# Performance work log

Hardware: AMD Instinct MI355X
Metric: run time of the kernel (lower is better)

The kernel has to match this reference:

```python
import jax, jax.numpy as jnp
import numpy as np

N, E, H, C = 100000, 1600000, 64, 40

def _mlp(h, w1, b1, w2, b2):
    return jax.nn.relu(h @ w1 + b1) @ w2 + b2

def setup_inputs() -> dict:
    key = jax.random.key(0)
    ks = jax.random.split(key, 16)
    def w(k, shape, fan_in):
        return jax.random.normal(k, shape, jnp.float32) / np.sqrt(fan_in)
    return {
        "x": jax.random.normal(ks[0], (N, H), jnp.float32),
        "edge_index": jax.random.randint(ks[1], (2, E), 0, N, jnp.int64),
        "edge_attr": jax.random.normal(ks[2], (E, 1), jnp.float32),
        # edge_mlp: Linear(1,H) -> ReLU -> Linear(H,H)
        "e_w1": w(ks[3], (1, H), 1), "e_b1": jnp.zeros((H,), jnp.float32),
        "e_w2": w(ks[4], (H, H), H), "e_b2": jnp.zeros((H,), jnp.float32),
        # conv1 update MLP + eps
        "eps1": jnp.zeros((), jnp.float32),
        "m1_w1": w(ks[5], (H, H), H), "m1_b1": jnp.zeros((H,), jnp.float32),
        "m1_w2": w(ks[6], (H, H), H), "m1_b2": jnp.zeros((H,), jnp.float32),
        # conv2 update MLP + eps
        "eps2": jnp.zeros((), jnp.float32),
        "m2_w1": w(ks[7], (H, H), H), "m2_b1": jnp.zeros((H,), jnp.float32),
        "m2_w2": w(ks[8], (H, H), H), "m2_b2": jnp.zeros((H,), jnp.float32),
        # classifier
        "lin_w": w(ks[9], (H, C), H), "lin_b": jnp.zeros((C,), jnp.float32),
    }

def reference(x, edge_index, edge_attr, e_w1, e_b1, e_w2, e_b2,
              eps1, m1_w1, m1_b1, m1_w2, m1_b2,
              eps2, m2_w1, m2_b1, m2_w2, m2_b2, lin_w, lin_b):
    n = x.shape[0]
    src, dst = edge_index[0], edge_index[1]
    edge_emb = _mlp(edge_attr, e_w1, e_b1, e_w2, e_b2)  # [E, H]

    def gine_conv(h, eps, w1, b1, w2, b2):
        msg = jax.nn.relu(h[src] + edge_emb)                 # gather + fuse  [E, H]
        aggr = jax.ops.segment_sum(msg, dst, num_segments=n) # scatter-add   [N, H]
        return _mlp((1.0 + eps) * h + aggr, w1, b1, w2, b2)

    h = jax.nn.relu(gine_conv(x, eps1, m1_w1, m1_b1, m1_w2, m1_b2))
    # dropout is identity in eval mode
    h = jax.nn.relu(gine_conv(h, eps2, m2_w1, m2_b1, m2_w2, m2_b2))
    return jax.nn.log_softmax(h @ lin_w + lin_b, axis=1)
```

## Files before the change

### kernel.cpp

```cpp
#include <hip/hip_runtime.h>
#include <hip/hip_bf16.h>
#include <stdint.h>


typedef unsigned int uint32;
typedef unsigned short ushort16;
typedef __attribute__((ext_vector_type(8))) short bf16x8;
typedef __attribute__((ext_vector_type(4))) float f32x4;

#define BKT_SHIFT 9
#define BKT_SIZE 512
#define BKT_MASK 511
#define BSPLIT 4

static __device__ __forceinline__ unsigned short f2bf(float f) {
  __hip_bfloat16 h = __float2bfloat16(f);
  return *reinterpret_cast<unsigned short*>(&h);
}
static __device__ __forceinline__ float bf2f(unsigned short u) {
  return __uint_as_float(((uint32)u) << 16);
}

static __device__ __forceinline__ bool detect_is64(const uint32* ei, int E, int tid, int* sflag) {
  if (tid < 64) {
    int lim = (E < 64) ? E : 64;
    int nz = (tid < lim) ? (ei[2 * (size_t)tid + 1] != 0u) : 0;
    nz = __any(nz);
    if (tid == 0) *sflag = !nz;
  }
  __syncthreads();
  return *sflag != 0;
}

__global__ __launch_bounds__(256) void k_setup_cast_count(
    const float* __restrict__ w1, const float* __restrict__ b1,
    const float* __restrict__ w2, const float* __restrict__ b2,
    float* __restrict__ tsS, uint32* __restrict__ ABp,
    const float* __restrict__ xin, ushort16* __restrict__ xb, int n4,
    const uint32* __restrict__ ei, int* __restrict__ hist1, int E, int KB) {
  __shared__ float w2s[64 * 64];
  __shared__ float b2s[64];
  __shared__ float w1s[64], b1s[64], ts[64];
  __shared__ int rs[64], ms[64], vs[64];
  __shared__ int h[1024];
  __shared__ int sIs64;
  const int tid = threadIdx.x;
  const int CB = (n4 + 255) >> 8;
  if (blockIdx.x >= (uint32)(65 + CB)) {
    const int b = blockIdx.x - (65 + CB);
    for (int i = tid; i < 1024; i += 256) h[i] = 0;
    bool is64 = detect_is64(ei, E, tid, &sIs64);
    for (int i = b * 256 + tid; i < E; i += KB * 256) {
      int dst = is64 ? (int)ei[2 * ((size_t)E + i)] : (int)ei[(size_t)E + i];
      atomicAdd(&h[dst >> BKT_SHIFT], 1);
    }
    __syncthreads();
    for (int i = tid; i < 1024; i += 256)
      if (h[i]) atomicAdd(&hist1[i], h[i]);
    return;
  }
  if (blockIdx.x >= 65) {
    int i = (blockIdx.x - 65) * 256 + tid;
    if (i < n4) {
      float4 v = ((const float4*)xin)[i];
      ushort4 o;
      o.x = f2bf(v.x); o.y = f2bf(v.y); o.z = f2bf(v.z); o.w = f2bf(v.w);
      ((ushort4*)xb)[i] = o;
    }
    return;
  }
  const int p = blockIdx.x;
  {
    const float4* g4 = (const float4*)w2;
    float4* s4 = (float4*)w2s;
    for (int i = tid; i < 64 * 16; i += 256) s4[i] = g4[i];
    if (tid < 64) b2s[tid] = b2[tid];
  }
  if (tid < 64) {
    float w = w1[tid], b = b1[tid];
    w1s[tid] = w; b1s[tid] = b;
    int v = (w != 0.0f);
    vs[tid] = v;
    ts[tid] = v ? (-b / w) : 0.0f;
  }
  __syncthreads();
  if (tid < 64) {
    float tk = ts[tid];
    int r = 0, m = 0;
    for (int k = 0; k < 64; ++k) if (vs[k]) { r += (ts[k] < tk) ? 1 : 0; m += (ts[k] == tk) ? 1 : 0; }
    rs[tid] = r; ms[tid] = m;
    if (p == 0) {
      int pos;
      if (vs[tid]) {
        int c = 0;
        for (int j = 0; j < 64; ++j)
          if (vs[j] && (ts[j] < tk || (ts[j] == tk && j < tid))) c++;
        pos = c;
      } else {
        int c = 0;
        for (int j = 0; j < 64; ++j) if (vs[j]) c++;
        for (int j = 0; j < tid; ++j) if (!vs[j]) c++;
        pos = c;
      }
      tsS[pos] = vs[tid] ? tk : __builtin_inff();
    }
  }
  __syncthreads();
  if (tid < 64) {
    const int j = tid;
    float accA = 0.0f, accB = b2s[j];
    for (int k = 0; k < 64; ++k) {
      bool act;
      if (vs[k]) act = (w1s[k] > 0.0f) ? (p >= rs[k] + ms[k]) : (p <= rs[k]);
      else       act = (b1s[k] > 0.0f);
      if (act) { float wv = w2s[k * 64 + j]; accA = fmaf(w1s[k], wv, accA); accB = fmaf(b1s[k], wv, accB); }
    }
    ABp[p * 64 + j] = (uint32)f2bf(accA) | ((uint32)f2bf(accB) << 16);
  }
}

static __device__ __forceinline__ int scan_hist(const int* __restrict__ hist1,
                                                int* bo, int* psum, int tid) {
  int v0 = hist1[tid * 4 + 0], v1 = hist1[tid * 4 + 1];
  int v2 = hist1[tid * 4 + 2], v3 = hist1[tid * 4 + 3];
  int sum = v0 + v1 + v2 + v3;
  psum[tid] = sum;
  __syncthreads();
  for (int d = 1; d < 256; d <<= 1) {
    int add = (tid >= d) ? psum[tid - d] : 0;
    __syncthreads();
    psum[tid] += add;
    __syncthreads();
  }
  int run = psum[tid] - sum;
  bo[tid * 4 + 0] = run; run += v0;
  bo[tid * 4 + 1] = run; run += v1;
  bo[tid * 4 + 2] = run; run += v2;
  bo[tid * 4 + 3] = run; run += v3;
  int total = psum[255];
  __syncthreads();
  return total;
}


__global__ __launch_bounds__(256) void k_bpart(
    const uint32* __restrict__ ei, const float* __restrict__ ea,
    const float* __restrict__ tsSg, const int* __restrict__ hist1,
    int* __restrict__ bCur,
    int2* __restrict__ stage, unsigned short* __restrict__ dstw, int E) {
  __shared__ int cnt[1024];
  __shared__ int bo[1024];
  __shared__ int psum[256];
  __shared__ float tss[64];
  __shared__ int sIs64;
  __shared__ int2 sspay[2048];
  __shared__ uint32 ssmeta[2048];
  const int tid = threadIdx.x;
  for (int i = tid; i < 1024; i += 256) cnt[i] = 0;
  if (tid >= 64 && tid < 128) tss[tid - 64] = tsSg[tid - 64];
  bool is64 = detect_is64(ei, E, tid, &sIs64);
  scan_hist(hist1, bo, psum, tid);
  const int base0 = blockIdx.x * 2048;
  int dstv[8], srcv[8], rk[8];
  float av[8];
#pragma unroll
  for (int e = 0; e < 8; ++e) {
    int idx = base0 + e * 256 + tid;
    if (idx < E) {
      int src, dst;
      if (is64) { src = (int)ei[2 * (size_t)idx]; dst = (int)ei[2 * ((size_t)E + idx)]; }
      else      { src = (int)ei[(size_t)idx];     dst = (int)ei[(size_t)E + idx]; }
      dstv[e] = dst; srcv[e] = src; av[e] = ea[idx];
      rk[e] = atomicAdd(&cnt[dst >> BKT_SHIFT], 1);
    } else dstv[e] = -1;
  }
  __syncthreads();
  for (int b = tid; b < 1024; b += 256) {
    int c = cnt[b];
    if (c) bo[b] = bo[b] + atomicAdd(&bCur[b], c);
  }
  int v0 = cnt[tid * 4 + 0], v1 = cnt[tid * 4 + 1];
  int v2 = cnt[tid * 4 + 2], v3 = cnt[tid * 4 + 3];
  int lsum = v0 + v1 + v2 + v3;
  __syncthreads();
  psum[tid] = lsum;
  __syncthreads();
  for (int d = 1; d < 256; d <<= 1) {
    int add = (tid >= d) ? psum[tid - d] : 0;
    __syncthreads();
    psum[tid] += add;
    __syncthreads();
  }
  int lrun = psum[tid] - lsum;
  cnt[tid * 4 + 0] = lrun; lrun += v0;
  cnt[tid * 4 + 1] = lrun; lrun += v1;
  cnt[tid * 4 + 2] = lrun; lrun += v2;
  cnt[tid * 4 + 3] = lrun;
  const int totloc = psum[255];
  __syncthreads();
#pragma unroll
  for (int e = 0; e < 8; ++e) {
    if (dstv[e] < 0) continue;
    float a = av[e];
    int p = 0;
#pragma unroll
    for (int s = 32; s > 0; s >>= 1) if (tss[p + s - 1] < a) p += s;
    if (tss[p] < a) ++p;
    const int b = dstv[e] >> BKT_SHIFT;
    const int slot = cnt[b] + rk[e];
    const int gd = bo[b] + rk[e];
    sspay[slot] = make_int2(srcv[e] | (p << 20), __float_as_int(a));
    ssmeta[slot] = (uint32)gd | ((uint32)(dstv[e] & BKT_MASK) << 21);
  }
  __syncthreads();
  for (int j = tid; j < totloc; j += 256) {
    uint32 m = ssmeta[j];
    int gd = (int)(m & 0x1FFFFFu);
    stage[gd] = sspay[j];
    dstw[gd] = (unsigned short)(m >> 21);
  }
}

__global__ __launch_bounds__(256) void k_blocal(
    const int* __restrict__ hist1, const int2* __restrict__ stage,
    const unsigned short* __restrict__ dstw,
    int* __restrict__ offs, int2* __restrict__ pay, int N) {
  __shared__ int bo[1024];
  __shared__ int psum[256];
  __shared__ int h[512], cur[512], ps2[256];
  const int tid = threadIdx.x;
  const int b = blockIdx.x >> 2;
  const int sub = blockIdx.x & 3;
  const int nbkt = (int)gridDim.x >> 2;
  int Etot = scan_hist(hist1, bo, psum, tid);
  const int s = bo[b];
  const int e2 = (b == nbkt - 1) ? Etot : bo[b + 1];
  if (b == 0 && sub == 0 && tid == 0) offs[N] = Etot;
  h[tid] = 0; h[tid + 256] = 0;
  __syncthreads();
  for (int j = s + tid; j < e2; j += 256) atomicAdd(&h[dstw[j]], 1);
  __syncthreads();
  int a0 = h[2 * tid], a1 = h[2 * tid + 1];
  ps2[tid] = a0 + a1;
  __syncthreads();
  for (int d = 1; d < 256; d <<= 1) {
    int add = (tid >= d) ? ps2[tid - d] : 0;
    __syncthreads();
    ps2[tid] += add;
    __syncthreads();
  }
  int ex = s + ps2[tid] - (a0 + a1);
  cur[2 * tid] = ex;
  cur[2 * tid + 1] = ex + a0;
  {
    int local = 2 * tid;
    if ((local >> 7) == sub) {
      int nd0 = b * BKT_SIZE + local;
      if (nd0 < N) offs[nd0] = ex;
      if (nd0 + 1 < N) offs[nd0 + 1] = ex + a0;
    }
  }
  __syncthreads();
  const int lo = sub << 7, hi = lo + 128;
  for (int j = s + tid; j < e2; j += 256) {
    int d = dstw[j];
    if (d >= lo && d < hi) {
      int pos = atomicAdd(&cur[d], 1);
      pay[pos] = stage[j];
    }
  }
}


#define EDGE8_LOAD(ib, qx, av)                                   \
  _Pragma("unroll")                                              \
  for (int t = 0; t < 8; ++t) {                                  \
    int2 q_ = pay[(ib) + t];                                     \
    qx[t] = (uint32)__builtin_amdgcn_readfirstlane(q_.x);        \
    av[t] = (uint32)__builtin_amdgcn_readfirstlane(q_.y);        \
  }

#define EDGE8_GATHER(qx, xv, ab)                                 \
  _Pragma("unroll")                                              \
  for (int t = 0; t < 8; ++t) {                                  \
    xv[t] = bf2f(xb[(size_t)(qx[t] & 0xFFFFFu) * 64u + lane]);   \
    ab[t] = ABs[(qx[t] >> 20) * 64u + lane];                     \
  }

#define EDGE8_ACC(av, xv, ab, acc)                               \
  _Pragma("unroll")                                              \
  for (int t = 0; t < 8; ++t)                                    \
    acc += fmaxf(fmaf(__uint_as_float(av[t]),                    \
                      __uint_as_float(ab[t] << 16),              \
                      __uint_as_float(ab[t] & 0xffff0000u)) + xv[t], 0.0f);

#define EDGE1(ib, acc) do {                                      \
    int2 q_ = pay[(ib)];                                         \
    uint32 qx_ = (uint32)__builtin_amdgcn_readfirstlane(q_.x);   \
    uint32 av_ = (uint32)__builtin_amdgcn_readfirstlane(q_.y);   \
    float xv_ = bf2f(xb[(size_t)(qx_ & 0xFFFFFu) * 64u + lane]); \
    uint32 ab_ = ABs[(qx_ >> 20) * 64u + lane];                  \
    acc += fmaxf(fmaf(__uint_as_float(av_),                      \
                      __uint_as_float(ab_ << 16),                \
                      __uint_as_float(ab_ & 0xffff0000u)) + xv_, 0.0f); \
  } while (0)

__global__ __launch_bounds__(512, 8) void k_conv(
    const unsigned short* __restrict__ xb,
    const int* __restrict__ offs, const int2* __restrict__ pay,
    const uint32* __restrict__ ABp, const float* __restrict__ epsp,
    unsigned short* __restrict__ uout, int n) {
  __shared__ uint32 ABs[65 * 64];
  {
    const uint4* g4 = (const uint4*)ABp;
    uint4* s4 = (uint4*)ABs;
    for (int i = threadIdx.x; i < 65 * 16; i += 512) s4[i] = g4[i];
  }
  __syncthreads();
  const int lane = threadIdx.x & 63;
  const int wid = __builtin_amdgcn_readfirstlane((int)(threadIdx.x >> 6));
  const float scale = 1.0f + epsp[0];
  const int npair = (n + 1) >> 1;
  for (int w = blockIdx.x * 8 + wid; w < npair; w += gridDim.x * 8) {
    const int ndA = __builtin_amdgcn_readfirstlane(w * 2);
    const bool hasB = (ndA + 1) < n;
    const int sA = offs[ndA];
    const int eA = offs[ndA + 1];
    const int eB = hasB ? offs[ndA + 2] : eA;
    float accA = 0.0f, accB = 0.0f;
    int iA = sA, iB = eA;
    while (iA + 7 < eA && iB + 7 < eB) {
      const int ia = __builtin_amdgcn_readfirstlane(iA);
      const int ib = __builtin_amdgcn_readfirstlane(iB);
      uint32 qxA[8], avA[8], qxB[8], avB[8];
      EDGE8_LOAD(ia, qxA, avA);
      EDGE8_LOAD(ib, qxB, avB);
      float xvA[8], xvB[8];
      uint32 abA[8], abB[8];
      EDGE8_GATHER(qxA, xvA, abA);
      EDGE8_GATHER(qxB, xvB, abB);
      EDGE8_ACC(avA, xvA, abA, accA);
      EDGE8_ACC(avB, xvB, abB, accB);
      iA += 8; iB += 8;
    }
    while (iA + 7 < eA) {
      const int ia = __builtin_amdgcn_readfirstlane(iA);
      uint32 qx[8], av[8];
      EDGE8_LOAD(ia, qx, av);
      float xv[8]; uint32 ab[8];
      EDGE8_GATHER(qx, xv, ab);
      EDGE8_ACC(av, xv, ab, accA);
      iA += 8;
    }
    while (iB + 7 < eB) {
      const int ib = __builtin_amdgcn_readfirstlane(iB);
      uint32 qx[8], av[8];
      EDGE8_LOAD(ib, qx, av);
      float xv[8]; uint32 ab[8];
      EDGE8_GATHER(qx, xv, ab);
      EDGE8_ACC(av, xv, ab, accB);
      iB += 8;
    }
    while (iA < eA && iB < eB) {
      const int ia = __builtin_amdgcn_readfirstlane(iA);
      const int ib = __builtin_amdgcn_readfirstlane(iB);
      int2 qa = pay[ia];
      int2 qb = pay[ib];
      uint32 qxa = (uint32)__builtin_amdgcn_readfirstlane(qa.x);
      uint32 ava = (uint32)__builtin_amdgcn_readfirstlane(qa.y);
      uint32 qxb = (uint32)__builtin_amdgcn_readfirstlane(qb.x);
      uint32 avb = (uint32)__builtin_amdgcn_readfirstlane(qb.y);
      float xva = bf2f(xb[(size_t)(qxa & 0xFFFFFu) * 64u + lane]);
      float xvb = bf2f(xb[(size_t)(qxb & 0xFFFFFu) * 64u + lane]);
      uint32 aba = ABs[(qxa >> 20) * 64u + lane];
      uint32 abb = ABs[(qxb >> 20) * 64u + lane];
      accA += fmaxf(fmaf(__uint_as_float(ava), __uint_as_float(aba << 16),
                         __uint_as_float(aba & 0xffff0000u)) + xva, 0.0f);
      accB += fmaxf(fmaf(__uint_as_float(avb), __uint_as_float(abb << 16),
                         __uint_as_float(abb & 0xffff0000u)) + xvb, 0.0f);
      ++iA; ++iB;
    }
    while (iA < eA) { EDGE1(__builtin_amdgcn_readfirstlane(iA), accA); ++iA; }
    while (iB < eB) { EDGE1(__builtin_amdgcn_readfirstlane(iB), accB); ++iB; }
    float xsA = bf2f(xb[(size_t)ndA * 64 + lane]);
    uout[(size_t)ndA * 64 + lane] = f2bf(fmaf(scale, xsA, accA));
    if (hasB) {
      float xsB = bf2f(xb[((size_t)ndA + 1) * 64 + lane]);
      uout[((size_t)ndA + 1) * 64 + lane] = f2bf(fmaf(scale, xsB, accB));
    }
  }
}

template <int OUTW>
static __device__ __forceinline__ bf16x8 load_bfrag(const float* __restrict__ W,
                                                    int hh, int q, int ncol, bool valid) {
  bf16x8 f;
#pragma unroll
  for (int j = 0; j < 8; ++j) {
    int k = hh * 32 + q * 8 + j;
    f[j] = valid ? (short)f2bf(W[k * OUTW + ncol]) : (short)0;
  }
  return f;
}

#define MFMA_BF16(A, B, C) __builtin_amdgcn_mfma_f32_16x16x32_bf16((A), (B), (C), 0, 0, 0)

__global__ __launch_bounds__(256) void k_mlp1(
    const unsigned short* __restrict__ uin, unsigned short* __restrict__ houtb,
    const float* __restrict__ W1, const float* __restrict__ B1,
    const float* __restrict__ W2, const float* __restrict__ B2, int n) {
  __shared__ unsigned short T[4][16 * 72];
  const int lane = threadIdx.x & 63;
  const int wid = threadIdx.x >> 6;
  const int cl = lane & 15;
  const int q = lane >> 4;
  bf16x8 w1f[4][2], w2f[4][2];
  float b1v[4], b2v[4];
#pragma unroll
  for (int t = 0; t < 4; ++t) {
#pragma unroll
    for (int hh = 0; hh < 2; ++hh) {
      w1f[t][hh] = load_bfrag<64>(W1, hh, q, t * 16 + cl, true);
      w2f[t][hh] = load_bfrag<64>(W2, hh, q, t * 16 + cl, true);
    }
    b1v[t] = B1[t * 16 + cl];
    b2v[t] = B2[t * 16 + cl];
  }
  unsigned short* Tw = T[wid];
  for (int node0 = blockIdx.x * 64 + wid * 16; node0 < n; node0 += gridDim.x * 64) {
    const unsigned short* ub = uin + (size_t)(node0 + cl) * 64;
    bf16x8 au0 = *(const bf16x8*)(ub + q * 8);
    bf16x8 au1 = *(const bf16x8*)(ub + 32 + q * 8);
#pragma unroll
    for (int t = 0; t < 4; ++t) {
      f32x4 acc = {b1v[t], b1v[t], b1v[t], b1v[t]};
      acc = MFMA_BF16(au0, w1f[t][0], acc);
      acc = MFMA_BF16(au1, w1f[t][1], acc);
#pragma unroll
      for (int r = 0; r < 4; ++r)
        Tw[(q * 4 + r) * 72 + t * 16 + cl] = f2bf(fmaxf(acc[r], 0.0f));
    }
    bf16x8 ah0 = *(const bf16x8*)&Tw[cl * 72 + q * 8];
    bf16x8 ah1 = *(const bf16x8*)&Tw[cl * 72 + 32 + q * 8];
#pragma unroll
    for (int t = 0; t < 4; ++t) {
      f32x4 acc = {b2v[t], b2v[t], b2v[t], b2v[t]};
      acc = MFMA_BF16(ah0, w2f[t][0], acc);
      acc = MFMA_BF16(ah1, w2f[t][1], acc);
#pragma unroll
      for (int r = 0; r < 4; ++r)
        Tw[(q * 4 + r) * 72 + t * 16 + cl] = f2bf(fmaxf(acc[r], 0.0f));
    }
    int m2 = lane >> 2, pt = lane & 3;
    if (node0 + m2 < n) {
      bf16x8 c0 = *(const bf16x8*)&Tw[m2 * 72 + pt * 16];
      bf16x8 c1 = *(const bf16x8*)&Tw[m2 * 72 + pt * 16 + 8];
      unsigned short* ob = houtb + (size_t)(node0 + m2) * 64 + pt * 16;
      *(bf16x8*)ob = c0;
      *(bf16x8*)(ob + 8) = c1;
    }
  }
}

__global__ __launch_bounds__(256) void k_mlp_cls(
    const unsigned short* __restrict__ uin,
    const float* __restrict__ W1, const float* __restrict__ B1,
    const float* __restrict__ W2, const float* __restrict__ B2,
    const float* __restrict__ LW, const float* __restrict__ LB,
    float* __restrict__ out, int n) {
  __shared__ unsigned short T[4][16 * 72];
  __shared__ float L[4][16 * 52];
  const int lane = threadIdx.x & 63;
  const int wid = threadIdx.x >> 6;
  const int cl = lane & 15;
  const int q = lane >> 4;
  bf16x8 w1f[4][2], w2f[4][2], lwf[3][2];
  float b1v[4], b2v[4], lbv[3];
#pragma unroll
  for (int t = 0; t < 4; ++t) {
#pragma unroll
    for (int hh = 0; hh < 2; ++hh) {
      w1f[t][hh] = load_bfrag<64>(W1, hh, q, t * 16 + cl, true);
      w2f[t][hh] = load_bfrag<64>(W2, hh, q, t * 16 + cl, true);
    }
    b1v[t] = B1[t * 16 + cl];
    b2v[t] = B2[t * 16 + cl];
  }
#pragma unroll
  for (int t = 0; t < 3; ++t) {
    bool valid = (t * 16 + cl) < 40;
#pragma unroll
    for (int hh = 0; hh < 2; ++hh)
      lwf[t][hh] = load_bfrag<40>(LW, hh, q, valid ? (t * 16 + cl) : 0, valid);
    lbv[t] = valid ? LB[t * 16 + cl] : 0.0f;
  }
  unsigned short* Tw = T[wid];
  float* Lw = L[wid];
  for (int node0 = blockIdx.x * 64 + wid * 16; node0 < n; node0 += gridDim.x * 64) {
    const unsigned short* ub = uin + (size_t)(node0 + cl) * 64;
    bf16x8 au0 = *(const bf16x8*)(ub + q * 8);
    bf16x8 au1 = *(const bf16x8*)(ub + 32 + q * 8);
#pragma unroll
    for (int t = 0; t < 4; ++t) {
      f32x4 acc = {b1v[t], b1v[t], b1v[t], b1v[t]};
      acc = MFMA_BF16(au0, w1f[t][0], acc);
      acc = MFMA_BF16(au1, w1f[t][1], acc);
#pragma unroll
      for (int r = 0; r < 4; ++r)
        Tw[(q * 4 + r) * 72 + t * 16 + cl] = f2bf(fmaxf(acc[r], 0.0f));
    }
    bf16x8 ah0 = *(const bf16x8*)&Tw[cl * 72 + q * 8];
    bf16x8 ah1 = *(const bf16x8*)&Tw[cl * 72 + 32 + q * 8];
#pragma unroll
    for (int t = 0; t < 4; ++t) {
      f32x4 acc = {b2v[t], b2v[t], b2v[t], b2v[t]};
      acc = MFMA_BF16(ah0, w2f[t][0], acc);
      acc = MFMA_BF16(ah1, w2f[t][1], acc);
#pragma unroll
      for (int r = 0; r < 4; ++r)
        Tw[(q * 4 + r) * 72 + t * 16 + cl] = f2bf(fmaxf(acc[r], 0.0f));
    }
    bf16x8 g0 = *(const bf16x8*)&Tw[cl * 72 + q * 8];
    bf16x8 g1 = *(const bf16x8*)&Tw[cl * 72 + 32 + q * 8];
#pragma unroll
    for (int t = 0; t < 3; ++t) {
      f32x4 acc = {lbv[t], lbv[t], lbv[t], lbv[t]};
      acc = MFMA_BF16(g0, lwf[t][0], acc);
      acc = MFMA_BF16(g1, lwf[t][1], acc);
#pragma unroll
      for (int r = 0; r < 4; ++r)
        Lw[(q * 4 + r) * 52 + t * 16 + cl] = acc[r];
    }
    int m3 = lane >> 2, j3 = lane & 3;
    float lg[10];
#pragma unroll
    for (int i = 0; i < 10; ++i) lg[i] = Lw[m3 * 52 + j3 * 10 + i];
    float mx = lg[0];
#pragma unroll
    for (int i = 1; i < 10; ++i) mx = fmaxf(mx, lg[i]);
    mx = fmaxf(mx, __shfl_xor(mx, 1));
    mx = fmaxf(mx, __shfl_xor(mx, 2));
    float se = 0.0f;
#pragma unroll
    for (int i = 0; i < 10; ++i) se += __expf(lg[i] - mx);
    se += __shfl_xor(se, 1);
    se += __shfl_xor(se, 2);
    float lse = mx + __logf(se);
    if (node0 + m3 < n) {
      float* o = out + (size_t)(node0 + m3) * 40 + j3 * 10;
#pragma unroll
      for (int i = 0; i < 10; ++i) o[i] = lg[i] - lse;
    }
  }
}

extern "C" void kernel_launch(void* const* d_in, const int* in_sizes, int n_in,
                              void* d_out, int out_size, void* d_ws, size_t ws_size,
                              hipStream_t stream) {
  (void)n_in; (void)out_size; (void)ws_size;
  const float* x     = (const float*)d_in[0];
  const uint32* ei   = (const uint32*)d_in[1];
  const float* eattr = (const float*)d_in[2];
  const float* e_w1 = (const float*)d_in[3];
  const float* e_b1 = (const float*)d_in[4];
  const float* e_w2 = (const float*)d_in[5];
  const float* e_b2 = (const float*)d_in[6];
  const float* eps1 = (const float*)d_in[7];
  const float* m1w1 = (const float*)d_in[8];
  const float* m1b1 = (const float*)d_in[9];
  const float* m1w2 = (const float*)d_in[10];
  const float* m1b2 = (const float*)d_in[11];
  const float* eps2 = (const float*)d_in[12];
  const float* m2w1 = (const float*)d_in[13];
  const float* m2b1 = (const float*)d_in[14];
  const float* m2w2 = (const float*)d_in[15];
  const float* m2b2 = (const float*)d_in[16];
  const float* linw = (const float*)d_in[17];
  const float* linb = (const float*)d_in[18];

  const int N = in_sizes[0] / 64;
  const int E = in_sizes[1] / 2;
  const int NBKT = (N + BKT_SIZE - 1) >> BKT_SHIFT;

  char* ws = (char*)d_ws;
  size_t off = 0;
  auto alloc = [&](size_t bytes, size_t align) {
    off = (off + align - 1) & ~(align - 1);
    size_t r = off; off += bytes; return r;
  };
  size_t oT    = alloc(64 * 4, 64);
  size_t oAB   = alloc(65 * 64 * 4, 64);
  size_t oHC   = alloc(2048 * 4, 128);
  size_t oOffs = alloc(((size_t)N + 1) * 4, 128);
  size_t oPay  = alloc((size_t)E * 8, 256);
  size_t oXb   = alloc((size_t)N * 64 * 2 + 32768, 256);
  size_t oU    = alloc((size_t)N * 64 * 2 + 32768, 1024);
  size_t oStg  = alloc((size_t)E * 8, 256);
  size_t oDw   = alloc((size_t)E * 2, 256);

  float*  tsS  = (float*)(ws + oT);
  uint32* ABp  = (uint32*)(ws + oAB);
  int*    h1   = (int*)(ws + oHC);
  int*    bCur = (int*)(ws + oHC + 1024 * 4);
  int*    offs = (int*)(ws + oOffs);
  int2*   pay  = (int2*)(ws + oPay);
  ushort16* xb = (ushort16*)(ws + oXb);
  ushort16* ubuf = (ushort16*)(ws + oU);
  int2*   stage = (int2*)(ws + oStg);
  unsigned short* dstw = (unsigned short*)(ws + oDw);

  hipMemsetAsync(ws + oHC, 0, 2048 * 4, stream);

  const int n4 = N * 64 / 4;
  const int CB = (n4 + 255) / 256;
  const int PB = (E + 2047) / 2048;
  const int KB = 1024;
  const int MB = (N + 127) / 128;

  k_setup_cast_count<<<65 + CB + KB, 256, 0, stream>>>(
      e_w1, e_b1, e_w2, e_b2, tsS, ABp, x, xb, n4, ei, h1, E, KB);
  k_bpart<<<PB, 256, 0, stream>>>(ei, eattr, tsS, h1, bCur, stage, dstw, E);
  k_blocal<<<NBKT * BSPLIT, 256, 0, stream>>>(h1, stage, dstw, offs, pay, N);
  k_conv<<<1024, 512, 0, stream>>>((const unsigned short*)xb, offs, pay, ABp, eps1, ubuf, N);
  k_mlp1<<<MB, 256, 0, stream>>>((const unsigned short*)ubuf, (unsigned short*)xb,
                                 m1w1, m1b1, m1w2, m1b2, N);
  k_conv<<<1024, 512, 0, stream>>>((const unsigned short*)xb, offs, pay, ABp, eps2, ubuf, N);
  k_mlp_cls<<<MB, 256, 0, stream>>>((const unsigned short*)ubuf,
                                    m2w1, m2b1, m2w2, m2b2, linw, linb,
                                    (float*)d_out, N);
}
```

Measured before the change: 319.9 us.

## Fuse CSR-build setup, histogram, partition and local sort into one cooperative kernel

Replaces the memset plus three preprocessing kernels (setup/cast/count, bucket partition, bucket-local sort) with one persistent cooperative kernel. Its phases are separated by grid-wide syncs and walk the work with grid-stride loops. The goal is to remove launch gaps and the separate memset. In exchange it pays for grid.sync barriers, caps the grid at the number of co-resident blocks, and falls back to the old path when occupancy is too low.

```diff
diff --git a/kernel.cpp b/kernel.cpp
--- a/kernel.cpp
+++ b/kernel.cpp
@@ -1,6 +1,9 @@
 #include <hip/hip_runtime.h>
+#include <hip/hip_cooperative_groups.h>
 #include <hip/hip_bf16.h>
 #include <stdint.h>
+
+namespace cg = cooperative_groups;
 
 
 typedef unsigned int uint32;
@@ -30,6 +33,260 @@
   }
   __syncthreads();
   return *sflag != 0;
+}
+
+static __device__ __forceinline__ int scan_hist_p(const int* __restrict__ hist1,
+                                                  int* bo, int* psum, int tid) {
+  int v0 = hist1[tid * 4 + 0], v1 = hist1[tid * 4 + 1];
+  int v2 = hist1[tid * 4 + 2], v3 = hist1[tid * 4 + 3];
+  int sum = v0 + v1 + v2 + v3;
+  psum[tid] = sum;
+  __syncthreads();
+  for (int d = 1; d < 256; d <<= 1) {
+    int add = (tid >= d) ? psum[tid - d] : 0;
+    __syncthreads();
+    psum[tid] += add;
+    __syncthreads();
+  }
+  int run = psum[tid] - sum;
+  bo[tid * 4 + 0] = run; run += v0;
+  bo[tid * 4 + 1] = run; run += v1;
+  bo[tid * 4 + 2] = run; run += v2;
+  bo[tid * 4 + 3] = run; run += v3;
+  int total = psum[255];
+  __syncthreads();
+  return total;
+}
+
+__global__ __launch_bounds__(256, 4) void k_csr(
+    const float* __restrict__ w1, const float* __restrict__ b1,
+    const float* __restrict__ w2, const float* __restrict__ b2,
+    float* __restrict__ tsS, uint32* __restrict__ ABp,
+    const float* __restrict__ xin, ushort16* __restrict__ xb, int n4,
+    const uint32* __restrict__ ei, const float* __restrict__ ea,
+    int* __restrict__ hist1, int* __restrict__ bCur,
+    int2* __restrict__ stage, unsigned short* __restrict__ dstw,
+    int* __restrict__ offs, int2* __restrict__ pay, int N, int E) {
+  cg::grid_group grid = cg::this_grid();
+  const int tid = threadIdx.x;
+  const int bid = blockIdx.x;
+  const int G = (int)gridDim.x;
+  __shared__ __align__(16) char smem[34816];
+
+  if (bid < 65) {
+    float* w2s = (float*)smem;
+    float* b2s = (float*)(smem + 16384);
+    float* w1s = (float*)(smem + 16640);
+    float* b1s = (float*)(smem + 16896);
+    float* ts  = (float*)(smem + 17152);
+    int* rs = (int*)(smem + 17408);
+    int* ms = (int*)(smem + 17664);
+    int* vs = (int*)(smem + 17920);
+    const int p = bid;
+    {
+      const float4* g4 = (const float4*)w2;
+      float4* s4 = (float4*)w2s;
+      for (int i = tid; i < 64 * 16; i += 256) s4[i] = g4[i];
+      if (tid < 64) b2s[tid] = b2[tid];
+    }
+    if (tid < 64) {
+      float w = w1[tid], b = b1[tid];
+      w1s[tid] = w; b1s[tid] = b;
+      int v = (w != 0.0f);
+      vs[tid] = v;
+      ts[tid] = v ? (-b / w) : 0.0f;
+    }
+    __syncthreads();
+    if (tid < 64) {
+      float tk = ts[tid];
+      int r = 0, m = 0;
+      for (int k = 0; k < 64; ++k) if (vs[k]) { r += (ts[k] < tk) ? 1 : 0; m += (ts[k] == tk) ? 1 : 0; }
+      rs[tid] = r; ms[tid] = m;
+      if (p == 0) {
+        int pos;
+        if (vs[tid]) {
+          int c = 0;
+          for (int j = 0; j < 64; ++j)
+            if (vs[j] && (ts[j] < tk || (ts[j] == tk && j < tid))) c++;
+          pos = c;
+        } else {
+          int c = 0;
+          for (int j = 0; j < 64; ++j) if (vs[j]) c++;
+          for (int j = 0; j < tid; ++j) if (!vs[j]) c++;
+          pos = c;
+        }
+        tsS[pos] = vs[tid] ? tk : __builtin_inff();
+      }
+    }
+    __syncthreads();
+    if (tid < 64) {
+      const int j = tid;
+      float accA = 0.0f, accB = b2s[j];
+      for (int k = 0; k < 64; ++k) {
+        bool act;
+        if (vs[k]) act = (w1s[k] > 0.0f) ? (p >= rs[k] + ms[k]) : (p <= rs[k]);
+        else       act = (b1s[k] > 0.0f);
+        if (act) { float wv = w2s[k * 64 + j]; accA = fmaf(w1s[k], wv, accA); accB = fmaf(b1s[k], wv, accB); }
+      }
+      ABp[p * 64 + j] = (uint32)f2bf(accA) | ((uint32)f2bf(accB) << 16);
+    }
+  } else {
+    if (bid == G - 1) {
+      for (int i = tid; i < 2048; i += 256) hist1[i] = 0;
+    }
+    for (int i = (bid - 65) * 256 + tid; i < n4; i += (G - 65) * 256) {
+      float4 v = ((const float4*)xin)[i];
+      ushort4 o;
+      o.x = f2bf(v.x); o.y = f2bf(v.y); o.z = f2bf(v.z); o.w = f2bf(v.w);
+      ((ushort4*)xb)[i] = o;
+    }
+  }
+  grid.sync();
+
+  {
+    int* h = (int*)smem;
+    int* sflag = (int*)(smem + 4096);
+    for (int i = tid; i < 1024; i += 256) h[i] = 0;
+    bool is64 = detect_is64(ei, E, tid, sflag);
+    for (int i = bid * 256 + tid; i < E; i += G * 256) {
+      int dst = is64 ? (int)ei[2 * ((size_t)E + i)] : (int)ei[(size_t)E + i];
+      atomicAdd(&h[dst >> BKT_SHIFT], 1);
+    }
+    __syncthreads();
+    for (int i = tid; i < 1024; i += 256)
+      if (h[i]) atomicAdd(&hist1[i], h[i]);
+  }
+  grid.sync();
+
+  {
+    int* cnt = (int*)smem;
+    int* bo = (int*)(smem + 4096);
+    int* psum = (int*)(smem + 8192);
+    float* tss = (float*)(smem + 9216);
+    int* sflag = (int*)(smem + 9472);
+    int2* sspay = (int2*)(smem + 9728);
+    uint32* ssmeta = (uint32*)(smem + 26112);
+    if (tid >= 64 && tid < 128) tss[tid - 64] = tsS[tid - 64];
+    bool is64 = detect_is64(ei, E, tid, sflag);
+    const int PB = (E + 2047) >> 11;
+    for (int c = bid; c < PB; c += G) {
+      for (int i = tid; i < 1024; i += 256) cnt[i] = 0;
+      scan_hist_p(hist1, bo, psum, tid);
+      const int base0 = c * 2048;
+      int dstv[8], srcv[8], rk[8];
+      float av[8];
+#pragma unroll
+      for (int e = 0; e < 8; ++e) {
+        int idx = base0 + e * 256 + tid;
+        if (idx < E) {
+          int src, dst;
+          if (is64) { src = (int)ei[2 * (size_t)idx]; dst = (int)ei[2 * ((size_t)E + idx)]; }
+          else      { src = (int)ei[(size_t)idx];     dst = (int)ei[(size_t)E + idx]; }
+          dstv[e] = dst; srcv[e] = src; av[e] = ea[idx];
+          rk[e] = atomicAdd(&cnt[dst >> BKT_SHIFT], 1);
+        } else dstv[e] = -1;
+      }
+      __syncthreads();
+      for (int b = tid; b < 1024; b += 256) {
+        int cc = cnt[b];
+        if (cc) bo[b] = bo[b] + atomicAdd(&bCur[b], cc);
+      }
+      int v0 = cnt[tid * 4 + 0], v1 = cnt[tid * 4 + 1];
+      int v2 = cnt[tid * 4 + 2], v3 = cnt[tid * 4 + 3];
+      int lsum = v0 + v1 + v2 + v3;
+      __syncthreads();
+      psum[tid] = lsum;
+      __syncthreads();
+      for (int d = 1; d < 256; d <<= 1) {
+        int add = (tid >= d) ? psum[tid - d] : 0;
+        __syncthreads();
+        psum[tid] += add;
+        __syncthreads();
+      }
+      int lrun = psum[tid] - lsum;
+      cnt[tid * 4 + 0] = lrun; lrun += v0;
+      cnt[tid * 4 + 1] = lrun; lrun += v1;
+      cnt[tid * 4 + 2] = lrun; lrun += v2;
+      cnt[tid * 4 + 3] = lrun;
+      const int totloc = psum[255];
+      __syncthreads();
+#pragma unroll
+      for (int e = 0; e < 8; ++e) {
+        if (dstv[e] < 0) continue;
+        float a = av[e];
+        int p = 0;
+#pragma unroll
+        for (int s = 32; s > 0; s >>= 1) if (tss[p + s - 1] < a) p += s;
+        if (tss[p] < a) ++p;
+        const int b = dstv[e] >> BKT_SHIFT;
+        const int slot = cnt[b] + rk[e];
+        const int gd = bo[b] + rk[e];
+        sspay[slot] = make_int2(srcv[e] | (p << 20), __float_as_int(a));
+        ssmeta[slot] = (uint32)gd | ((uint32)(dstv[e] & BKT_MASK) << 21);
+      }
+      __syncthreads();
+      for (int j = tid; j < totloc; j += 256) {
+        uint32 m = ssmeta[j];
+        int gd = (int)(m & 0x1FFFFFu);
+        stage[gd] = sspay[j];
+        dstw[gd] = (unsigned short)(m >> 21);
+      }
+      __syncthreads();
+    }
+  }
+  grid.sync();
+
+  {
+    int* bo = (int*)smem;
+    int* psum = (int*)(smem + 4096);
+    int* h = (int*)(smem + 5120);
+    int* cur = (int*)(smem + 7168);
+    int* ps2 = (int*)(smem + 9216);
+    const int nbkt = (N + BKT_SIZE - 1) >> BKT_SHIFT;
+    const int S = nbkt * BSPLIT;
+    for (int s = bid; s < S; s += G) {
+      const int b = s >> 2;
+      const int sub = s & 3;
+      int Etot = scan_hist_p(hist1, bo, psum, tid);
+      const int sB = bo[b];
+      const int e2 = (b == nbkt - 1) ? Etot : bo[b + 1];
+      if (s == 0 && tid == 0) offs[N] = Etot;
+      h[tid] = 0; h[tid + 256] = 0;
+      __syncthreads();
+      for (int j = sB + tid; j < e2; j += 256) atomicAdd(&h[dstw[j]], 1);
+      __syncthreads();
+      int a0 = h[2 * tid], a1 = h[2 * tid + 1];
+      ps2[tid] = a0 + a1;
+      __syncthreads();
+      for (int d = 1; d < 256; d <<= 1) {
+        int add = (tid >= d) ? ps2[tid - d] : 0;
+        __syncthreads();
+        ps2[tid] += add;
+        __syncthreads();
+      }
+      int ex = sB + ps2[tid] - (a0 + a1);
+      cur[2 * tid] = ex;
+      cur[2 * tid + 1] = ex + a0;
+      {
+        int local = 2 * tid;
+        if ((local >> 7) == sub) {
+          int nd0 = b * BKT_SIZE + local;
+          if (nd0 < N) offs[nd0] = ex;
+          if (nd0 + 1 < N) offs[nd0 + 1] = ex + a0;
+        }
+      }
+      __syncthreads();
+      const int lo = sub << 7, hi = lo + 128;
+      for (int j = sB + tid; j < e2; j += 256) {
+        int d = dstw[j];
+        if (d >= lo && d < hi) {
+          int pos = atomicAdd(&cur[d], 1);
+          pay[pos] = stage[j];
+        }
+      }
+      __syncthreads();
+    }
+  }
 }
 
 __global__ __launch_bounds__(256) void k_setup_cast_count(
@@ -119,30 +376,6 @@
   }
 }
 
-static __device__ __forceinline__ int scan_hist(const int* __restrict__ hist1,
-                                                int* bo, int* psum, int tid) {
-  int v0 = hist1[tid * 4 + 0], v1 = hist1[tid * 4 + 1];
-  int v2 = hist1[tid * 4 + 2], v3 = hist1[tid * 4 + 3];
-  int sum = v0 + v1 + v2 + v3;
-  psum[tid] = sum;
-  __syncthreads();
-  for (int d = 1; d < 256; d <<= 1) {
-    int add = (tid >= d) ? psum[tid - d] : 0;
-    __syncthreads();
-    psum[tid] += add;
-    __syncthreads();
-  }
-  int run = psum[tid] - sum;
-  bo[tid * 4 + 0] = run; run += v0;
-  bo[tid * 4 + 1] = run; run += v1;
-  bo[tid * 4 + 2] = run; run += v2;
-  bo[tid * 4 + 3] = run; run += v3;
-  int total = psum[255];
-  __syncthreads();
-  return total;
-}
-
-
 __global__ __launch_bounds__(256) void k_bpart(
     const uint32* __restrict__ ei, const float* __restrict__ ea,
     const float* __restrict__ tsSg, const int* __restrict__ hist1,
@@ -159,7 +392,7 @@
   for (int i = tid; i < 1024; i += 256) cnt[i] = 0;
   if (tid >= 64 && tid < 128) tss[tid - 64] = tsSg[tid - 64];
   bool is64 = detect_is64(ei, E, tid, &sIs64);
-  scan_hist(hist1, bo, psum, tid);
+  scan_hist_p(hist1, bo, psum, tid);
   const int base0 = blockIdx.x * 2048;
   int dstv[8], srcv[8], rk[8];
   float av[8];
@@ -232,7 +465,7 @@
   const int b = blockIdx.x >> 2;
   const int sub = blockIdx.x & 3;
   const int nbkt = (int)gridDim.x >> 2;
-  int Etot = scan_hist(hist1, bo, psum, tid);
+  int Etot = scan_hist_p(hist1, bo, psum, tid);
   const int s = bo[b];
   const int e2 = (b == nbkt - 1) ? Etot : bo[b + 1];
   if (b == 0 && sub == 0 && tid == 0) offs[N] = Etot;
@@ -270,7 +503,6 @@
     }
   }
 }
-
 
 #define EDGE8_LOAD(ib, qx, av)                                   \
   _Pragma("unroll")                                              \
@@ -609,18 +841,43 @@
   int2*   stage = (int2*)(ws + oStg);
   unsigned short* dstw = (unsigned short*)(ws + oDw);
 
-  hipMemsetAsync(ws + oHC, 0, 2048 * 4, stream);
-
   const int n4 = N * 64 / 4;
   const int CB = (n4 + 255) / 256;
   const int PB = (E + 2047) / 2048;
   const int KB = 1024;
   const int MB = (N + 127) / 128;
 
-  k_setup_cast_count<<<65 + CB + KB, 256, 0, stream>>>(
-      e_w1, e_b1, e_w2, e_b2, tsS, ABp, x, xb, n4, ei, h1, E, KB);
-  k_bpart<<<PB, 256, 0, stream>>>(ei, eattr, tsS, h1, bCur, stage, dstw, E);
-  k_blocal<<<NBKT * BSPLIT, 256, 0, stream>>>(h1, stage, dstw, offs, pay, N);
+  static int g_coopG = -2;
+  if (g_coopG == -2) {
+    int mb = 0;
+    hipError_t err = hipOccupancyMaxActiveBlocksPerMultiprocessor(&mb, k_csr, 256, 0);
+    if (err != hipSuccess) mb = 0;
+    int g = mb * 256;
+    if (g > 1024) g = 1024;
+    g_coopG = (g >= 512) ? g : -1;
+  }
+
+  if (g_coopG > 0) {
+    int Nv = N, Ev = E, n4v = n4;
+    void* args[] = {
+      (void*)&e_w1, (void*)&e_b1, (void*)&e_w2, (void*)&e_b2,
+      (void*)&tsS, (void*)&ABp,
+      (void*)&x, (void*)&xb, (void*)&n4v,
+      (void*)&ei, (void*)&eattr,
+      (void*)&h1, (void*)&bCur,
+      (void*)&stage, (void*)&dstw,
+      (void*)&offs, (void*)&pay, (void*)&Nv, (void*)&Ev
+    };
+    hipLaunchCooperativeKernel((const void*)k_csr, dim3(g_coopG), dim3(256),
+                               args, 0, stream);
+  } else {
+    hipMemsetAsync(ws + oHC, 0, 2048 * 4, stream);
+    k_setup_cast_count<<<65 + CB + KB, 256, 0, stream>>>(
+        e_w1, e_b1, e_w2, e_b2, tsS, ABp, x, xb, n4, ei, h1, E, KB);
+    k_bpart<<<PB, 256, 0, stream>>>(ei, eattr, tsS, h1, bCur, stage, dstw, E);
+    k_blocal<<<NBKT * BSPLIT, 256, 0, stream>>>(h1, stage, dstw, offs, pay, N);
+  }
+
   k_conv<<<1024, 512, 0, stream>>>((const unsigned short*)xb, offs, pay, ABp, eps1, ubuf, N);
   k_mlp1<<<MB, 256, 0, stream>>>((const unsigned short*)ubuf, (unsigned short*)xb,
                                  m1w1, m1b1, m1w2, m1b2, N);
```

Result: slower. 683.5 us (+113.7%).

## Fuse GINE aggregation with following MLP into one kernel per layer

Applied to the files above, without the earlier changes.

Merges each conv aggregation kernel with the following MLP kernel. Every wave now aggregates 16 nodes, writes the results to shared memory, and runs the MFMA MLP on them directly. This removes the round trip of the intermediate u buffer through global memory and saves two launches. In exchange, register pressure rises, the launch bound drops to 4 blocks per CU, and each block now does one tile instead of grid-striding.

```diff
diff --git a/kernel.cpp b/kernel.cpp
--- a/kernel.cpp
+++ b/kernel.cpp
@@ -142,7 +142,6 @@
   return total;
 }
 
-
 __global__ __launch_bounds__(256) void k_bpart(
     const uint32* __restrict__ ei, const float* __restrict__ ea,
     const float* __restrict__ tsSg, const int* __restrict__ hist1,
@@ -271,7 +270,6 @@
   }
 }
 
-
 #define EDGE8_LOAD(ib, qx, av)                                   \
   _Pragma("unroll")                                              \
   for (int t = 0; t < 8; ++t) {                                  \
@@ -305,111 +303,99 @@
                       __uint_as_float(ab_ & 0xffff0000u)) + xv_, 0.0f); \
   } while (0)
 
-__global__ __launch_bounds__(512, 8) void k_conv(
+static __device__ __forceinline__ void conv_pair(
+    const unsigned short* __restrict__ xb, const int* __restrict__ offs,
+    const int2* __restrict__ pay, const uint32* ABs, const int lane,
+    const int ndA, const bool hasB, float& accA, float& accB) {
+  const int sA = offs[ndA];
+  const int eA = offs[ndA + 1];
+  const int eB = hasB ? offs[ndA + 2] : eA;
+  accA = 0.0f; accB = 0.0f;
+  int iA = sA, iB = eA;
+  while (iA + 7 < eA && iB + 7 < eB) {
+    const int ia = __builtin_amdgcn_readfirstlane(iA);
+    const int ib = __builtin_amdgcn_readfirstlane(iB);
+    uint32 qxA[8], avA[8], qxB[8], avB[8];
+    EDGE8_LOAD(ia, qxA, avA);
+    EDGE8_LOAD(ib, qxB, avB);
+    float xvA[8], xvB[8];
+    uint32 abA[8], abB[8];
+    EDGE8_GATHER(qxA, xvA, abA);
+    EDGE8_GATHER(qxB, xvB, abB);
+    EDGE8_ACC(avA, xvA, abA, accA);
+    EDGE8_ACC(avB, xvB, abB, accB);
+    iA += 8; iB += 8;
+  }
+  while (iA + 7 < eA) {
+    const int ia = __builtin_amdgcn_readfirstlane(iA);
+    uint32 qx[8], av[8];
+    EDGE8_LOAD(ia, qx, av);
+    float xv[8]; uint32 ab[8];
+    EDGE8_GATHER(qx, xv, ab);
+    EDGE8_ACC(av, xv, ab, accA);
+    iA += 8;
+  }
+  while (iB + 7 < eB) {
+    const int ib = __builtin_amdgcn_readfirstlane(iB);
+    uint32 qx[8], av[8];
+    EDGE8_LOAD(ib, qx, av);
+    float xv[8]; uint32 ab[8];
+    EDGE8_GATHER(qx, xv, ab);
+    EDGE8_ACC(av, xv, ab, accB);
+    iB += 8;
+  }
+  while (iA < eA && iB < eB) {
+    const int ia = __builtin_amdgcn_readfirstlane(iA);
+    const int ib = __builtin_amdgcn_readfirstlane(iB);
+    int2 qa = pay[ia];
+    int2 qb = pay[ib];
+    uint32 qxa = (uint32)__builtin_amdgcn_readfirstlane(qa.x);
+    uint32 ava = (uint32)__builtin_amdgcn_readfirstlane(qa.y);
+    uint32 qxb = (uint32)__builtin_amdgcn_readfirstlane(qb.x);
+    uint32 avb = (uint32)__builtin_amdgcn_readfirstlane(qb.y);
+    float xva = bf2f(xb[(size_t)(qxa & 0xFFFFFu) * 64u + lane]);
+    float xvb = bf2f(xb[(size_t)(qxb & 0xFFFFFu) * 64u + lane]);
+    uint32 aba = ABs[(qxa >> 20) * 64u + lane];
+    uint32 abb = ABs[(qxb >> 20) * 64u + lane];
+    accA += fmaxf(fmaf(__uint_as_float(ava), __uint_as_float(aba << 16),
+                       __uint_as_float(aba & 0xffff0000u)) + xva, 0.0f);
+    accB += fmaxf(fmaf(__uint_as_float(avb), __uint_as_float(abb << 16),
+                       __uint_as_float(abb & 0xffff0000u)) + xvb, 0.0f);
+    ++iA; ++iB;
+  }
+  while (iA < eA) { EDGE1(__builtin_amdgcn_readfirstlane(iA), accA); ++iA; }
+  while (iB < eB) { EDGE1(__builtin_amdgcn_readfirstlane(iB), accB); ++iB; }
+}
+
+template <int OUTW>
+static __device__ __forceinline__ bf16x8 load_bfrag(const float* __restrict__ W,
+                                                    int hh, int q, int ncol, bool valid) {
+  bf16x8 f;
+#pragma unroll
+  for (int j = 0; j < 8; ++j) {
+    int k = hh * 32 + q * 8 + j;
+    f[j] = valid ? (short)f2bf(W[k * OUTW + ncol]) : (short)0;
+  }
+  return f;
+}
+
+#define MFMA_BF16(A, B, C) __builtin_amdgcn_mfma_f32_16x16x32_bf16((A), (B), (C), 0, 0, 0)
+
+__global__ __launch_bounds__(512, 4) void k_conv_mlp1(
     const unsigned short* __restrict__ xb,
     const int* __restrict__ offs, const int2* __restrict__ pay,
     const uint32* __restrict__ ABp, const float* __restrict__ epsp,
-    unsigned short* __restrict__ uout, int n) {
+    const float* __restrict__ W1, const float* __restrict__ B1,
+    const float* __restrict__ W2, const float* __restrict__ B2,
+    unsigned short* __restrict__ hout, int n) {
   __shared__ uint32 ABs[65 * 64];
+  __shared__ unsigned short Tu[8][16 * 72];
   {
     const uint4* g4 = (const uint4*)ABp;
     uint4* s4 = (uint4*)ABs;
     for (int i = threadIdx.x; i < 65 * 16; i += 512) s4[i] = g4[i];
   }
   __syncthreads();
-  const int lane = threadIdx.x & 63;
-  const int wid = __builtin_amdgcn_readfirstlane((int)(threadIdx.x >> 6));
-  const float scale = 1.0f + epsp[0];
-  const int npair = (n + 1) >> 1;
-  for (int w = blockIdx.x * 8 + wid; w < npair; w += gridDim.x * 8) {
-    const int ndA = __builtin_amdgcn_readfirstlane(w * 2);
-    const bool hasB = (ndA + 1) < n;
-    const int sA = offs[ndA];
-    const int eA = offs[ndA + 1];
-    const int eB = hasB ? offs[ndA + 2] : eA;
-    float accA = 0.0f, accB = 0.0f;
-    int iA = sA, iB = eA;
-    while (iA + 7 < eA && iB + 7 < eB) {
-      const int ia = __builtin_amdgcn_readfirstlane(iA);
-      const int ib = __builtin_amdgcn_readfirstlane(iB);
-      uint32 qxA[8], avA[8], qxB[8], avB[8];
-      EDGE8_LOAD(ia, qxA, avA);
-      EDGE8_LOAD(ib, qxB, avB);
-      float xvA[8], xvB[8];
-      uint32 abA[8], abB[8];
-      EDGE8_GATHER(qxA, xvA, abA);
-      EDGE8_GATHER(qxB, xvB, abB);
-      EDGE8_ACC(avA, xvA, abA, accA);
-      EDGE8_ACC(avB, xvB, abB, accB);
-      iA += 8; iB += 8;
-    }
-    while (iA + 7 < eA) {
-      const int ia = __builtin_amdgcn_readfirstlane(iA);
-      uint32 qx[8], av[8];
-      EDGE8_LOAD(ia, qx, av);
-      float xv[8]; uint32 ab[8];
-      EDGE8_GATHER(qx, xv, ab);
-      EDGE8_ACC(av, xv, ab, accA);
-      iA += 8;
-    }
-    while (iB + 7 < eB) {
-      const int ib = __builtin_amdgcn_readfirstlane(iB);
-      uint32 qx[8], av[8];
-      EDGE8_LOAD(ib, qx, av);
-      float xv[8]; uint32 ab[8];
-      EDGE8_GATHER(qx, xv, ab);
-      EDGE8_ACC(av, xv, ab, accB);
-      iB += 8;
-    }
-    while (iA < eA && iB < eB) {
-      const int ia = __builtin_amdgcn_readfirstlane(iA);
-      const int ib = __builtin_amdgcn_readfirstlane(iB);
-      int2 qa = pay[ia];
-      int2 qb = pay[ib];
-      uint32 qxa = (uint32)__builtin_amdgcn_readfirstlane(qa.x);
-      uint32 ava = (uint32)__builtin_amdgcn_readfirstlane(qa.y);
-      uint32 qxb = (uint32)__builtin_amdgcn_readfirstlane(qb.x);
-      uint32 avb = (uint32)__builtin_amdgcn_readfirstlane(qb.y);
-      float xva = bf2f(xb[(size_t)(qxa & 0xFFFFFu) * 64u + lane]);
-      float xvb = bf2f(xb[(size_t)(qxb & 0xFFFFFu) * 64u + lane]);
-      uint32 aba = ABs[(qxa >> 20) * 64u + lane];
-      uint32 abb = ABs[(qxb >> 20) * 64u + lane];
-      accA += fmaxf(fmaf(__uint_as_float(ava), __uint_as_float(aba << 16),
-                         __uint_as_float(aba & 0xffff0000u)) + xva, 0.0f);
-      accB += fmaxf(fmaf(__uint_as_float(avb), __uint_as_float(abb << 16),
-                         __uint_as_float(abb & 0xffff0000u)) + xvb, 0.0f);
-      ++iA; ++iB;
-    }
-    while (iA < eA) { EDGE1(__builtin_amdgcn_readfirstlane(iA), accA); ++iA; }
-    while (iB < eB) { EDGE1(__builtin_amdgcn_readfirstlane(iB), accB); ++iB; }
-    float xsA = bf2f(xb[(size_t)ndA * 64 + lane]);
-    uout[(size_t)ndA * 64 + lane] = f2bf(fmaf(scale, xsA, accA));
-    if (hasB) {
-      float xsB = bf2f(xb[((size_t)ndA + 1) * 64 + lane]);
-      uout[((size_t)ndA + 1) * 64 + lane] = f2bf(fmaf(scale, xsB, accB));
-    }
-  }
-}
-
-template <int OUTW>
-static __device__ __forceinline__ bf16x8 load_bfrag(const float* __restrict__ W,
-                                                    int hh, int q, int ncol, bool valid) {
-  bf16x8 f;
-#pragma unroll
-  for (int j = 0; j < 8; ++j) {
-    int k = hh * 32 + q * 8 + j;
-    f[j] = valid ? (short)f2bf(W[k * OUTW + ncol]) : (short)0;
-  }
-  return f;
-}
-
-#define MFMA_BF16(A, B, C) __builtin_amdgcn_mfma_f32_16x16x32_bf16((A), (B), (C), 0, 0, 0)
-
-__global__ __launch_bounds__(256) void k_mlp1(
-    const unsigned short* __restrict__ uin, unsigned short* __restrict__ houtb,
-    const float* __restrict__ W1, const float* __restrict__ B1,
-    const float* __restrict__ W2, const float* __restrict__ B2, int n) {
-  __shared__ unsigned short T[4][16 * 72];
   const int lane = threadIdx.x & 63;
   const int wid = threadIdx.x >> 6;
   const int cl = lane & 15;
@@ -426,11 +412,32 @@
     b1v[t] = B1[t * 16 + cl];
     b2v[t] = B2[t * 16 + cl];
   }
-  unsigned short* Tw = T[wid];
-  for (int node0 = blockIdx.x * 64 + wid * 16; node0 < n; node0 += gridDim.x * 64) {
-    const unsigned short* ub = uin + (size_t)(node0 + cl) * 64;
-    bf16x8 au0 = *(const bf16x8*)(ub + q * 8);
-    bf16x8 au1 = *(const bf16x8*)(ub + 32 + q * 8);
+  const float scale = 1.0f + epsp[0];
+  const int T = (n + 15) >> 4;
+  unsigned short* Tw = Tu[wid];
+  for (int t0 = blockIdx.x * 8 + wid; t0 < T; t0 += gridDim.x * 8) {
+    const int base = __builtin_amdgcn_readfirstlane(t0 << 4);
+    if (base + 16 > n) {
+#pragma unroll 1
+      for (int r = 0; r < 16; ++r)
+        if (base + r >= n) Tw[r * 72 + lane] = 0;
+    }
+#pragma unroll 1
+    for (int pp = 0; pp < 8; ++pp) {
+      const int ndA = base + 2 * pp;
+      if (ndA >= n) break;
+      const bool hasB = (ndA + 1) < n;
+      float accA, accB;
+      conv_pair(xb, offs, pay, ABs, lane, ndA, hasB, accA, accB);
+      float xsA = bf2f(xb[(size_t)ndA * 64 + lane]);
+      Tw[(2 * pp) * 72 + lane] = f2bf(fmaf(scale, xsA, accA));
+      if (hasB) {
+        float xsB = bf2f(xb[((size_t)ndA + 1) * 64 + lane]);
+        Tw[(2 * pp + 1) * 72 + lane] = f2bf(fmaf(scale, xsB, accB));
+      }
+    }
+    bf16x8 au0 = *(const bf16x8*)&Tw[cl * 72 + q * 8];
+    bf16x8 au1 = *(const bf16x8*)&Tw[cl * 72 + 32 + q * 8];
 #pragma unroll
     for (int t = 0; t < 4; ++t) {
       f32x4 acc = {b1v[t], b1v[t], b1v[t], b1v[t]};
@@ -452,24 +459,33 @@
         Tw[(q * 4 + r) * 72 + t * 16 + cl] = f2bf(fmaxf(acc[r], 0.0f));
     }
     int m2 = lane >> 2, pt = lane & 3;
-    if (node0 + m2 < n) {
+    if (base + m2 < n) {
       bf16x8 c0 = *(const bf16x8*)&Tw[m2 * 72 + pt * 16];
       bf16x8 c1 = *(const bf16x8*)&Tw[m2 * 72 + pt * 16 + 8];
-      unsigned short* ob = houtb + (size_t)(node0 + m2) * 64 + pt * 16;
+      unsigned short* ob = hout + (size_t)(base + m2) * 64 + pt * 16;
       *(bf16x8*)ob = c0;
       *(bf16x8*)(ob + 8) = c1;
     }
   }
 }
 
-__global__ __launch_bounds__(256) void k_mlp_cls(
-    const unsigned short* __restrict__ uin,
+__global__ __launch_bounds__(512, 4) void k_conv_mlp_cls(
+    const unsigned short* __restrict__ xb,
+    const int* __restrict__ offs, const int2* __restrict__ pay,
+    const uint32* __restrict__ ABp, const float* __restrict__ epsp,
     const float* __restrict__ W1, const float* __restrict__ B1,
     const float* __restrict__ W2, const float* __restrict__ B2,
     const float* __restrict__ LW, const float* __restrict__ LB,
     float* __restrict__ out, int n) {
-  __shared__ unsigned short T[4][16 * 72];
-  __shared__ float L[4][16 * 52];
+  __shared__ uint32 ABs[65 * 64];
+  __shared__ unsigned short Tu[8][16 * 72];
+  __shared__ float L[8][16 * 52];
+  {
+    const uint4* g4 = (const uint4*)ABp;
+    uint4* s4 = (uint4*)ABs;
+    for (int i = threadIdx.x; i < 65 * 16; i += 512) s4[i] = g4[i];
+  }
+  __syncthreads();
   const int lane = threadIdx.x & 63;
   const int wid = threadIdx.x >> 6;
   const int cl = lane & 15;
@@ -494,12 +510,33 @@
       lwf[t][hh] = load_bfrag<40>(LW, hh, q, valid ? (t * 16 + cl) : 0, valid);
     lbv[t] = valid ? LB[t * 16 + cl] : 0.0f;
   }
-  unsigned short* Tw = T[wid];
+  const float scale = 1.0f + epsp[0];
+  const int T = (n + 15) >> 4;
+  unsigned short* Tw = Tu[wid];
   float* Lw = L[wid];
-  for (int node0 = blockIdx.x * 64 + wid * 16; node0 < n; node0 += gridDim.x * 64) {
-    const unsigned short* ub = uin + (size_t)(node0 + cl) * 64;
-    bf16x8 au0 = *(const bf16x8*)(ub + q * 8);
-    bf16x8 au1 = *(const bf16x8*)(ub + 32 + q * 8);
+  for (int t0 = blockIdx.x * 8 + wid; t0 < T; t0 += gridDim.x * 8) {
+    const int base = __builtin_amdgcn_readfirstlane(t0 << 4);
+    if (base + 16 > n) {
+#pragma unroll 1
+      for (int r = 0; r < 16; ++r)
+        if (base + r >= n) Tw[r * 72 + lane] = 0;
+    }
+#pragma unroll 1
+    for (int pp = 0; pp < 8; ++pp) {
+      const int ndA = base + 2 * pp;
+      if (ndA >= n) break;
+      const bool hasB = (ndA + 1) < n;
+      float accA, accB;
+      conv_pair(xb, offs, pay, ABs, lane, ndA, hasB, accA, accB);
+      float xsA = bf2f(xb[(size_t)ndA * 64 + lane]);
+      Tw[(2 * pp) * 72 + lane] = f2bf(fmaf(scale, xsA, accA));
+      if (hasB) {
+        float xsB = bf2f(xb[((size_t)ndA + 1) * 64 + lane]);
+        Tw[(2 * pp + 1) * 72 + lane] = f2bf(fmaf(scale, xsB, accB));
+      }
+    }
+    bf16x8 au0 = *(const bf16x8*)&Tw[cl * 72 + q * 8];
+    bf16x8 au1 = *(const bf16x8*)&Tw[cl * 72 + 32 + q * 8];
 #pragma unroll
     for (int t = 0; t < 4; ++t) {
       f32x4 acc = {b1v[t], b1v[t], b1v[t], b1v[t]};
@@ -546,8 +583,8 @@
     se += __shfl_xor(se, 1);
     se += __shfl_xor(se, 2);
     float lse = mx + __logf(se);
-    if (node0 + m3 < n) {
-      float* o = out + (size_t)(node0 + m3) * 40 + j3 * 10;
+    if (base + m3 < n) {
+      float* o = out + (size_t)(base + m3) * 40 + j3 * 10;
 #pragma unroll
       for (int i = 0; i < 10; ++i) o[i] = lg[i] - lse;
     }
@@ -613,19 +650,18 @@
 
   const int n4 = N * 64 / 4;
   const int CB = (n4 + 255) / 256;
-  const int PB = (E + 2047) / 2048;
   const int KB = 1024;
-  const int MB = (N + 127) / 128;
+  const int T = (N + 15) / 16;
+  const int FB = (T + 7) / 8;
 
   k_setup_cast_count<<<65 + CB + KB, 256, 0, stream>>>(
       e_w1, e_b1, e_w2, e_b2, tsS, ABp, x, xb, n4, ei, h1, E, KB);
-  k_bpart<<<PB, 256, 0, stream>>>(ei, eattr, tsS, h1, bCur, stage, dstw, E);
+  k_bpart<<<(E + 2047) / 2048, 256, 0, stream>>>(ei, eattr, tsS, h1, bCur, stage, dstw, E);
   k_blocal<<<NBKT * BSPLIT, 256, 0, stream>>>(h1, stage, dstw, offs, pay, N);
-  k_conv<<<1024, 512, 0, stream>>>((const unsigned short*)xb, offs, pay, ABp, eps1, ubuf, N);
-  k_mlp1<<<MB, 256, 0, stream>>>((const unsigned short*)ubuf, (unsigned short*)xb,
-                                 m1w1, m1b1, m1w2, m1b2, N);
-  k_conv<<<1024, 512, 0, stream>>>((const unsigned short*)xb, offs, pay, ABp, eps2, ubuf, N);
-  k_mlp_cls<<<MB, 256, 0, stream>>>((const unsigned short*)ubuf,
-                                    m2w1, m2b1, m2w2, m2b2, linw, linb,
-                                    (float*)d_out, N);
-}
+  k_conv_mlp1<<<FB, 512, 0, stream>>>((const unsigned short*)xb, offs, pay, ABp, eps1,
+                                      m1w1, m1b1, m1w2, m1b2,
+                                      (unsigned short*)ubuf, N);
+  k_conv_mlp_cls<<<FB, 512, 0, stream>>>((const unsigned short*)ubuf, offs, pay, ABp, eps2,
+                                         m2w1, m2b1, m2w2, m2b2, linw, linb,
+                                         (float*)d_out, N);
+}
```

New measurement: 500.0 us. +56.3%, slower.
